# Performance work log

Hardware: AMD Instinct MI355X
Metric: run time of the kernel (lower is better)

## Reference

```python
import jax, jax.numpy as jnp
import numpy as np


def squash(x, axis=-1):
    # squared_norm * x / ((1 + squared_norm) * sqrt(squared_norm))
    sn = jnp.sum(x * x, axis=axis, keepdims=True)
    return sn * x / ((1.0 + sn) * jnp.sqrt(sn))


def conv2d(x, w, b, stride):
    out = jax.lax.conv_general_dilated(
        x, w, (stride, stride), 'VALID',
        dimension_numbers=('NCHW', 'OIHW', 'NCHW'))
    return out + b[None, :, None, None]


def setup_inputs() -> dict:
    key = jax.random.key(0)
    ks = jax.random.split(key, 8)
    B = 256
    s = 0.05
    data = jax.random.normal(ks[0], (B, 1, 28, 28), jnp.float32)
    conv_w = jax.random.normal(ks[1], (256, 1, 9, 9), jnp.float32) * s
    conv_b = jnp.zeros((256,), jnp.float32)
    pc_w = jax.random.normal(ks[2], (8, 32, 256, 9, 9), jnp.float32) * s  # 8 capsule convs
    pc_b = jnp.zeros((8, 32), jnp.float32)
    W = jax.random.normal(ks[3], (1, 1152, 10, 16, 8), jnp.float32)  # torch.randn init
    dec_w1 = jax.random.normal(ks[4], (512, 160), jnp.float32) * s
    dec_b1 = jnp.zeros((512,), jnp.float32)
    dec_w2 = jax.random.normal(ks[5], (1024, 512), jnp.float32) * s
    dec_b2 = jnp.zeros((1024,), jnp.float32)
    dec_w3 = jax.random.normal(ks[6], (784, 1024), jnp.float32) * s
    dec_b3 = jnp.zeros((784,), jnp.float32)
    return dict(data=data, conv_w=conv_w, conv_b=conv_b, pc_w=pc_w, pc_b=pc_b,
                W=W, dec_w1=dec_w1, dec_b1=dec_b1, dec_w2=dec_w2, dec_b2=dec_b2,
                dec_w3=dec_w3, dec_b3=dec_b3)


def reference(data, conv_w, conv_b, pc_w, pc_b, W,
              dec_w1, dec_b1, dec_w2, dec_b2, dec_w3, dec_b3):
    B = data.shape[0]
    # ConvLayer
    x = jax.nn.relu(conv2d(data, conv_w, conv_b, 1))        # [B,256,20,20]
    # PrimaryCaps: 8 separate convs == one conv with 8*32 output channels
    pw = pc_w.reshape(8 * 32, 256, 9, 9)
    pb = pc_b.reshape(8 * 32)
    u = conv2d(x, pw, pb, 2)                                # [B,256,6,6] == stack dim=1 of [B,8,32,6,6]
    u = u.reshape(B, 1152, 8)                               # matches torch .view(B, num_routes, -1)
    u = squash(u)                                           # over 8-dim capsule axis
    # DigitCaps: u_hat[b,r,c,o] = W[0,r,c,o,:] . u[b,r,:]
    u_hat = jnp.einsum('rcoi,bri->brco', W[0], u)           # [B,1152,10,16]
    b_ij = jnp.zeros((1, 1152, 10, 1), u_hat.dtype)         # shared across batch (as in torch)
    v_j = None
    for it in range(3):
        c = jax.nn.softmax(b_ij, axis=1)                    # softmax over routes
        s_j = jnp.sum(c * u_hat, axis=1, keepdims=True)     # [B,1,10,16]
        # NOTE: torch squash here acts on a trailing singleton dim -> elementwise
        # out = s^2 * s / ((1+s^2)*|s|) = s*|s|/(1+s^2)
        v_j = s_j * jnp.abs(s_j) / (1.0 + s_j * s_j)
        if it < 2:
            a = jnp.sum(u_hat * v_j, axis=3)                # agreement, [B,1152,10]
            b_ij = b_ij + jnp.mean(a, axis=0, keepdims=True)[..., None]
    output = v_j[:, 0, :, :, None]                          # [B,10,16,1] (v_j.squeeze(1) in torch layout)
    # Decoder
    classes = jnp.sqrt(jnp.sum(output ** 2, axis=2))        # [B,10,1]
    classes = jax.nn.softmax(classes, axis=0)               # dim=0 softmax (as in source)
    idx = jnp.argmax(classes[:, :, 0], axis=1)              # [B]
    masked = jnp.eye(10, dtype=output.dtype)[idx]           # [B,10]
    t = (output * masked[:, :, None, None]).reshape(B, -1)  # [B,160]
    h = jax.nn.relu(t @ dec_w1.T + dec_b1)
    h = jax.nn.relu(h @ dec_w2.T + dec_b2)
    recon = jax.nn.sigmoid(h @ dec_w3.T + dec_b3)
    reconstructions = recon.reshape(B, 1, 28, 28)
    return output, reconstructions, masked
```

## Files before the change

kernel.cpp:

```cpp
#include <hip/hip_runtime.h>
#include <math.h>

typedef __attribute__((ext_vector_type(8))) short short8;
typedef __attribute__((ext_vector_type(16))) float f32x16;
typedef unsigned short ushort_t;

static __device__ __forceinline__ unsigned short f2bf(float f) {
  unsigned int u = __float_as_uint(f);
  u += 0x7FFF + ((u >> 16) & 1);
  return (unsigned short)(u >> 16);
}
static __device__ __forceinline__ float bf2f(unsigned short h) {
  return __uint_as_float(((unsigned int)h) << 16);
}

__device__ __forceinline__ void gl2lds16(const void* g, void* l) {
  __builtin_amdgcn_global_load_lds(
      (const __attribute__((address_space(1))) unsigned int*)g,
      (__attribute__((address_space(3))) unsigned int*)l, 16, 0, 0);
}

__global__ __launch_bounds__(256) void acvt_kernel(const float* __restrict__ cw,
                                                   ushort_t* __restrict__ ah,
                                                   ushort_t* __restrict__ al) {
  int tid = blockIdx.x * 256 + threadIdx.x;
  if (tid >= 4608) return;
  int l = tid & 63;
  int ocg = (tid >> 6) & 7;
  int kc = tid >> 9;
  int oc = ocg * 32 + (l & 31);
  size_t obase = (size_t)tid * 8;
#pragma unroll
  for (int e = 0; e < 8; ++e) {
    int kwp = ((l >> 5) << 3) + e;
    float v = (kwp < 9) ? cw[oc * 81 + kc * 9 + kwp] : 0.f;
    unsigned short h = f2bf(v);
    ah[obase + e] = h;
    al[obase + e] = f2bf(v - bf2f(h));
  }
}

__global__ __launch_bounds__(256) void im2col_kernel(const float* __restrict__ data,
                                                     ushort_t* __restrict__ bh,
                                                     ushort_t* __restrict__ bl) {
  int idx16 = blockIdx.x * 256 + threadIdx.x;
  int kc = idx16 / 204800;
  int rem = idx16 - kc * 204800;
  int n = rem >> 1, half = rem & 1;
  int b = n / 400;
  int pos = n - b * 400;
  int ph = pos / 20, pw = pos - ph * 20;
  const float* src = data + b * 784 + (ph + kc) * 28 + pw + half * 8;
  size_t obase = (size_t)idx16 * 8;
#pragma unroll
  for (int e = 0; e < 8; ++e) {
    int kwp = half * 8 + e;
    float v = (kwp < 9) ? src[e] : 0.f;
    unsigned short h = f2bf(v);
    bh[obase + e] = h;
    bl[obase + e] = f2bf(v - bf2f(h));
  }
}

struct StageC {
  ushort_t ah[2][8][64][8];
  ushort_t al[2][8][64][8];
  ushort_t bh[2][2][64][8];
  ushort_t bl[2][2][64][8];
};
__global__ __launch_bounds__(256, 2) void cgemm_kernel(
    const ushort_t* __restrict__ Afh, const ushort_t* __restrict__ Afl,
    const ushort_t* __restrict__ Bfh, const ushort_t* __restrict__ Bfl,
    const float* __restrict__ cb, ushort_t* __restrict__ xTh,
    ushort_t* __restrict__ xTl) {
  __shared__ __align__(16) union { StageC st; float ep[256][33]; } L;
  const int t = threadIdx.x;
  const int l = t & 63;
  const int w = t >> 6;
  const int n0 = blockIdx.x * 64;

  f32x16 acc[2][2];
#pragma unroll
  for (int j = 0; j < 2; ++j)
#pragma unroll
    for (int nc = 0; nc < 2; ++nc)
#pragma unroll
      for (int r = 0; r < 16; ++r) acc[j][nc][r] = 0.f;

  auto stage = [&](int buf, int kc) {
#pragma unroll
    for (int q5 = 0; q5 < 5; ++q5) {
      int q = w * 5 + q5;
      if (q < 16) {
        int sp = q >> 3, ocg = q & 7;
        const ushort_t* src = (sp ? Afl : Afh) + ((size_t)(kc * 8 + ocg) * 64 + l) * 8;
        gl2lds16(src, sp ? &L.st.al[buf][ocg][0][0] : &L.st.ah[buf][ocg][0][0]);
      } else {
        int j = q - 16;
        int sp = j >> 1, nc = j & 1;
        const ushort_t* src =
            (sp ? Bfl : Bfh) +
            (((size_t)kc * 102400 + (n0 + nc * 32 + (l & 31))) * 2 + (l >> 5)) * 8;
        gl2lds16(src, sp ? &L.st.bl[buf][nc][0][0] : &L.st.bh[buf][nc][0][0]);
      }
    }
  };

  stage(0, 0);
  __syncthreads();
  int buf = 0;
  for (int kc = 0; kc < 9; ++kc) {
    if (kc < 8) stage(buf ^ 1, kc + 1);
    short8 a0h = *(const short8*)&L.st.ah[buf][2 * w + 0][l][0];
    short8 a1h = *(const short8*)&L.st.ah[buf][2 * w + 1][l][0];
    short8 a0l = *(const short8*)&L.st.al[buf][2 * w + 0][l][0];
    short8 a1l = *(const short8*)&L.st.al[buf][2 * w + 1][l][0];
#pragma unroll
    for (int nc = 0; nc < 2; ++nc) {
      short8 bh = *(const short8*)&L.st.bh[buf][nc][l][0];
      short8 bl = *(const short8*)&L.st.bl[buf][nc][l][0];
      acc[0][nc] = __builtin_amdgcn_mfma_f32_32x32x16_bf16(a0h, bh, acc[0][nc], 0, 0, 0);
      acc[0][nc] = __builtin_amdgcn_mfma_f32_32x32x16_bf16(a0h, bl, acc[0][nc], 0, 0, 0);
      acc[0][nc] = __builtin_amdgcn_mfma_f32_32x32x16_bf16(a0l, bh, acc[0][nc], 0, 0, 0);
      acc[1][nc] = __builtin_amdgcn_mfma_f32_32x32x16_bf16(a1h, bh, acc[1][nc], 0, 0, 0);
      acc[1][nc] = __builtin_amdgcn_mfma_f32_32x32x16_bf16(a1h, bl, acc[1][nc], 0, 0, 0);
      acc[1][nc] = __builtin_amdgcn_mfma_f32_32x32x16_bf16(a1l, bh, acc[1][nc], 0, 0, 0);
    }
    __syncthreads();
    buf ^= 1;
  }

  for (int nc = 0; nc < 2; ++nc) {
    __syncthreads();
#pragma unroll
    for (int j = 0; j < 2; ++j)
#pragma unroll
      for (int r = 0; r < 16; ++r) {
        int row = w * 64 + j * 32 + (r & 3) + 8 * (r >> 2) + ((l >> 5) << 2);
        L.ep[row][l & 31] = fmaxf(acc[j][nc][r] + cb[row], 0.f);
      }
    __syncthreads();
    int nl = t >> 3, ocr = (t & 7) * 32;
    size_t ng = (size_t)(n0 + nc * 32 + nl);
#pragma unroll
    for (int q8 = 0; q8 < 4; ++q8) {
      short8 sh, sl;
#pragma unroll
      for (int e = 0; e < 8; ++e) {
        float vv = L.ep[ocr + q8 * 8 + e][nl];
        unsigned short h = f2bf(vv);
        sh[e] = (short)h;
        sl[e] = (short)f2bf(vv - bf2f(h));
      }
      *(short8*)&xTh[ng * 256 + ocr + q8 * 8] = sh;
      *(short8*)&xTl[ng * 256 + ocr + q8 * 8] = sl;
    }
  }
}

__global__ __launch_bounds__(256) void wcvt_kernel(const float* __restrict__ pw,
                                                   ushort_t* __restrict__ ah,
                                                   ushort_t* __restrict__ al) {
  int tid = blockIdx.x * 256 + threadIdx.x;
  int l = tid & 63;
  int ocg = (tid >> 6) & 7;
  int kc = tid >> 9;
  int oc = ocg * 32 + (l & 31);
  size_t obase = (size_t)tid * 8;
#pragma unroll
  for (int e = 0; e < 8; ++e) {
    int k = kc * 16 + ((l >> 5) << 3) + e;
    int kh = k / 2304;
    int r = k - kh * 2304;
    int kw = r >> 8, ic = r & 255;
    float v = pw[((size_t)oc * 256 + ic) * 81 + kh * 9 + kw];
    unsigned short h = f2bf(v);
    ah[obase + e] = h;
    al[obase + e] = f2bf(v - bf2f(h));
  }
}

__global__ __launch_bounds__(256, 2) void pgemm_kernel(
    const ushort_t* __restrict__ Agh, const ushort_t* __restrict__ Agl,
    const ushort_t* __restrict__ Xh, const ushort_t* __restrict__ Xl,
    float* __restrict__ part) {
  __shared__ __align__(16) ushort_t sA[2][2][2][4][64][8];
  __shared__ __align__(16) ushort_t sB[2][2][2][4][64][8];
  const int t = threadIdx.x;
  const int l = t & 63;
  const int w = t >> 6;
  const int wm = w >> 1, wn = w & 1;
  const int m0 = blockIdx.y;
  const int n0 = blockIdx.x * 128;
  const int zk = blockIdx.z;
  const int kcb = zk * 162;

  int n = n0 + w * 32 + (l & 31);
  int b_ = n / 36;
  int pos = n - b_ * 36;
  int ph = pos / 6, pww = pos - ph * 6;
  size_t pbase = (((size_t)b_ * 20 + 2 * ph) * 20 + 2 * pww) * 256 + ((l >> 5) << 3);

  const int sw = w >> 1, klw = w & 1;
  const ushort_t* Asrc = sw ? Agl : Agh;
  const size_t aoff0 = (((size_t)(kcb + klw) * 8 + m0 * 4) * 64 + l) * 8;

  f32x16 acc[2][2];
#pragma unroll
  for (int j = 0; j < 2; ++j)
#pragma unroll
    for (int j2 = 0; j2 < 2; ++j2)
#pragma unroll
      for (int r = 0; r < 16; ++r) acc[j][j2][r] = 0.f;

  auto koff = [](int kc) {
    int kh = (unsigned)kc / 144u;
    int r = kc - kh * 144;
    return ((kh * 20 + (r >> 4)) << 8) + ((r & 15) << 4);
  };
  auto stage = [&](int buf, int step) {
    size_t ao = aoff0 + (size_t)step * 8192;
#pragma unroll
    for (int j = 0; j < 4; ++j)
      gl2lds16(Asrc + ao + j * 512, &sA[buf][sw][klw][j][0][0]);
    int kc0 = kcb + 2 * step;
    int o0 = koff(kc0), o1 = koff(kc0 + 1);
    gl2lds16(Xh + pbase + o0, &sB[buf][0][0][w][0][0]);
    gl2lds16(Xh + pbase + o1, &sB[buf][0][1][w][0][0]);
    gl2lds16(Xl + pbase + o0, &sB[buf][1][0][w][0][0]);
    gl2lds16(Xl + pbase + o1, &sB[buf][1][1][w][0][0]);
  };

  stage(0, 0);
  __syncthreads();
  int buf = 0;
  for (int step = 0; step < 81; ++step) {
    if (step + 1 < 81) stage(buf ^ 1, step + 1);
#pragma unroll
    for (int kl = 0; kl < 2; ++kl) {
      short8 a0h = *(const short8*)&sA[buf][0][kl][wm * 2 + 0][l][0];
      short8 a1h = *(const short8*)&sA[buf][0][kl][wm * 2 + 1][l][0];
      short8 a0l = *(const short8*)&sA[buf][1][kl][wm * 2 + 0][l][0];
      short8 a1l = *(const short8*)&sA[buf][1][kl][wm * 2 + 1][l][0];
      short8 b0h = *(const short8*)&sB[buf][0][kl][wn * 2 + 0][l][0];
      short8 b1h = *(const short8*)&sB[buf][0][kl][wn * 2 + 1][l][0];
      short8 b0l = *(const short8*)&sB[buf][1][kl][wn * 2 + 0][l][0];
      short8 b1l = *(const short8*)&sB[buf][1][kl][wn * 2 + 1][l][0];
      acc[0][0] = __builtin_amdgcn_mfma_f32_32x32x16_bf16(a0h, b0h, acc[0][0], 0, 0, 0);
      acc[0][0] = __builtin_amdgcn_mfma_f32_32x32x16_bf16(a0h, b0l, acc[0][0], 0, 0, 0);
      acc[0][0] = __builtin_amdgcn_mfma_f32_32x32x16_bf16(a0l, b0h, acc[0][0], 0, 0, 0);
      acc[0][1] = __builtin_amdgcn_mfma_f32_32x32x16_bf16(a0h, b1h, acc[0][1], 0, 0, 0);
      acc[0][1] = __builtin_amdgcn_mfma_f32_32x32x16_bf16(a0h, b1l, acc[0][1], 0, 0, 0);
      acc[0][1] = __builtin_amdgcn_mfma_f32_32x32x16_bf16(a0l, b1h, acc[0][1], 0, 0, 0);
      acc[1][0] = __builtin_amdgcn_mfma_f32_32x32x16_bf16(a1h, b0h, acc[1][0], 0, 0, 0);
      acc[1][0] = __builtin_amdgcn_mfma_f32_32x32x16_bf16(a1h, b0l, acc[1][0], 0, 0, 0);
      acc[1][0] = __builtin_amdgcn_mfma_f32_32x32x16_bf16(a1l, b0h, acc[1][0], 0, 0, 0);
      acc[1][1] = __builtin_amdgcn_mfma_f32_32x32x16_bf16(a1h, b1h, acc[1][1], 0, 0, 0);
      acc[1][1] = __builtin_amdgcn_mfma_f32_32x32x16_bf16(a1h, b1l, acc[1][1], 0, 0, 0);
      acc[1][1] = __builtin_amdgcn_mfma_f32_32x32x16_bf16(a1l, b1h, acc[1][1], 0, 0, 0);
    }
    __syncthreads();
    buf ^= 1;
  }

#pragma unroll
  for (int j = 0; j < 2; ++j)
#pragma unroll
    for (int j2 = 0; j2 < 2; ++j2) {
      int ocb = m0 * 128 + wm * 64 + j * 32;
      int nb = n0 + wn * 64 + j2 * 32 + (l & 31);
#pragma unroll
      for (int r = 0; r < 16; ++r) {
        int row = (r & 3) + 8 * (r >> 2) + ((l >> 5) << 2);
        part[((size_t)(zk * 256 + ocb + row)) * 9216 + nb] = acc[j][j2][r];
      }
    }
}

__global__ __launch_bounds__(256) void ured_kernel(const float* __restrict__ part,
                                                   const float* __restrict__ pb,
                                                   float* __restrict__ u) {
  int tid = blockIdx.x * 256 + threadIdx.x;
  int oc = tid / 9216;
  int n = tid - oc * 9216;
  float s = pb[oc];
#pragma unroll
  for (int z = 0; z < 8; ++z) s += part[((size_t)z * 256 + oc) * 9216 + n];
  int b = n / 36;
  int pos = n - b * 36;
  u[(size_t)b * 9216 + oc * 36 + pos] = s;
}

__global__ __launch_bounds__(256) void sqcvt_kernel(const float* __restrict__ u,
                                                    ushort_t* __restrict__ ubh,
                                                    ushort_t* __restrict__ ubl,
                                                    ushort_t* __restrict__ uth,
                                                    ushort_t* __restrict__ utl) {
  int kt = blockIdx.x, bt = blockIdx.y;
  int k0 = kt * 64, b0 = bt * 64;
  __shared__ ushort_t lh[64][66], ll_[64][66];
  int t = threadIdx.x;
#pragma unroll
  for (int jj = 0; jj < 2; ++jj) {
    int item = t + 256 * jj;
    int g = item & 7, bl = item >> 3;
    int b = b0 + bl, kb = k0 + g * 8;
    const float4* p4 = reinterpret_cast<const float4*>(u + (size_t)b * 9216 + kb);
    float4 v0 = p4[0], v1 = p4[1];
    float va[8] = {v0.x, v0.y, v0.z, v0.w, v1.x, v1.y, v1.z, v1.w};
    float sn = 0.f;
#pragma unroll
    for (int e = 0; e < 8; ++e) sn += va[e] * va[e];
    float f = sn / ((1.f + sn) * sqrtf(sn));
    short8 sh, sl;
#pragma unroll
    for (int e = 0; e < 8; ++e) {
      float vv = va[e] * f;
      unsigned short h = f2bf(vv);
      unsigned short lo = f2bf(vv - bf2f(h));
      sh[e] = (short)h;
      sl[e] = (short)lo;
      lh[g * 8 + e][bl] = h;
      ll_[g * 8 + e][bl] = lo;
    }
    *(short8*)&ubh[(size_t)b * 9216 + kb] = sh;
    *(short8*)&ubl[(size_t)b * 9216 + kb] = sl;
  }
  __syncthreads();
  int kl = t >> 2, br = (t & 3) * 16;
#pragma unroll
  for (int q = 0; q < 2; ++q) {
    short8 sh, sl;
#pragma unroll
    for (int e = 0; e < 8; ++e) {
      sh[e] = (short)lh[kl][br + q * 8 + e];
      sl[e] = (short)ll_[kl][br + q * 8 + e];
    }
    *(short8*)&uth[(size_t)(k0 + kl) * 256 + b0 + br + q * 8] = sh;
    *(short8*)&utl[(size_t)(k0 + kl) * 256 + b0 + br + q * 8] = sl;
  }
}

__global__ void zero_kernel(float* __restrict__ p, int n) {
  int i = blockIdx.x * 256 + threadIdx.x;
  if (i < n) p[i] = 0.f;
}

__global__ __launch_bounds__(256) void softmax_c_kernel(const float* __restrict__ bp,
                                                        float* __restrict__ c) {
  int cls = blockIdx.x;
  int t = threadIdx.x;
  __shared__ float red[256];
  float m = -1e30f;
  for (int r = t; r < 1152; r += 256) m = fmaxf(m, bp[r * 10 + cls]);
  red[t] = m;
  __syncthreads();
  for (int s = 128; s > 0; s >>= 1) {
    if (t < s) red[t] = fmaxf(red[t], red[t + s]);
    __syncthreads();
  }
  m = red[0];
  __syncthreads();
  float sum = 0.f;
  for (int r = t; r < 1152; r += 256) sum += expf(bp[r * 10 + cls] - m);
  red[t] = sum;
  __syncthreads();
  for (int s = 128; s > 0; s >>= 1) {
    if (t < s) red[t] += red[t + s];
    __syncthreads();
  }
  float den = red[0];
  for (int r = t; r < 1152; r += 256) c[r * 10 + cls] = expf(bp[r * 10 + cls] - m) / den;
}

__global__ __launch_bounds__(256) void wcb_kernel(const float* __restrict__ W,
                                                  const float* __restrict__ c,
                                                  ushort_t* __restrict__ wh,
                                                  ushort_t* __restrict__ wl) {
  int tid = blockIdx.x * 256 + threadIdx.x;
  int col = tid / 1152;
  int kg = tid - col * 1152;
  int cls = col >> 4, o = col & 15;
  float cc = c[kg * 10 + cls];
  const float4* wp = reinterpret_cast<const float4*>(W + (((size_t)kg * 10 + cls) * 16 + o) * 8);
  float4 w0 = wp[0], w1 = wp[1];
  float wa[8] = {w0.x, w0.y, w0.z, w0.w, w1.x, w1.y, w1.z, w1.w};
  short8 sh, sl;
#pragma unroll
  for (int e = 0; e < 8; ++e) {
    float vv = wa[e] * cc;
    unsigned short h = f2bf(vv);
    sh[e] = (short)h;
    sl[e] = (short)f2bf(vv - bf2f(h));
  }
  *(short8*)&wh[(size_t)col * 9216 + kg * 8] = sh;
  *(short8*)&wl[(size_t)col * 9216 + kg * 8] = sl;
}

__global__ __launch_bounds__(64, 1) void smfma_kernel(
    const ushort_t* __restrict__ ubh, const ushort_t* __restrict__ ubl,
    const ushort_t* __restrict__ wh, const ushort_t* __restrict__ wl,
    float* __restrict__ s_part) {
  int ks = blockIdx.x, bt = blockIdx.y;
  __shared__ __align__(16) ushort_t Ah[4][2][64][8], Al[4][2][64][8];
  __shared__ __align__(16) ushort_t Bh[4][5][64][8], Bl[4][5][64][8];
  int l = threadIdx.x;
  int k0 = ks * 64;
#pragma unroll
  for (int kc = 0; kc < 4; ++kc) {
#pragma unroll
    for (int mh = 0; mh < 2; ++mh) {
      size_t ao = (size_t)(bt * 64 + mh * 32 + (l & 31)) * 9216 + k0 + kc * 16 + ((l >> 5) << 3);
      gl2lds16(ubh + ao, &Ah[kc][mh][0][0]);
      gl2lds16(ubl + ao, &Al[kc][mh][0][0]);
    }
#pragma unroll
    for (int cf = 0; cf < 5; ++cf) {
      size_t bo = (size_t)(cf * 32 + (l & 31)) * 9216 + k0 + kc * 16 + ((l >> 5) << 3);
      gl2lds16(wh + bo, &Bh[kc][cf][0][0]);
      gl2lds16(wl + bo, &Bl[kc][cf][0][0]);
    }
  }
  __builtin_amdgcn_s_waitcnt(0);
  __syncthreads();
  f32x16 acc[2][5];
#pragma unroll
  for (int m = 0; m < 2; ++m)
#pragma unroll
    for (int cf = 0; cf < 5; ++cf)
#pragma unroll
      for (int r = 0; r < 16; ++r) acc[m][cf][r] = 0.f;
#pragma unroll
  for (int kc = 0; kc < 4; ++kc) {
    short8 a0h = *(const short8*)&Ah[kc][0][l][0];
    short8 a1h = *(const short8*)&Ah[kc][1][l][0];
    short8 a0l = *(const short8*)&Al[kc][0][l][0];
    short8 a1l = *(const short8*)&Al[kc][1][l][0];
#pragma unroll
    for (int cf = 0; cf < 5; ++cf) {
      short8 bh = *(const short8*)&Bh[kc][cf][l][0];
      short8 bl = *(const short8*)&Bl[kc][cf][l][0];
      acc[0][cf] = __builtin_amdgcn_mfma_f32_32x32x16_bf16(a0h, bh, acc[0][cf], 0, 0, 0);
      acc[0][cf] = __builtin_amdgcn_mfma_f32_32x32x16_bf16(a0h, bl, acc[0][cf], 0, 0, 0);
      acc[0][cf] = __builtin_amdgcn_mfma_f32_32x32x16_bf16(a0l, bh, acc[0][cf], 0, 0, 0);
      acc[1][cf] = __builtin_amdgcn_mfma_f32_32x32x16_bf16(a1h, bh, acc[1][cf], 0, 0, 0);
      acc[1][cf] = __builtin_amdgcn_mfma_f32_32x32x16_bf16(a1h, bl, acc[1][cf], 0, 0, 0);
      acc[1][cf] = __builtin_amdgcn_mfma_f32_32x32x16_bf16(a1l, bh, acc[1][cf], 0, 0, 0);
    }
  }
#pragma unroll
  for (int mh = 0; mh < 2; ++mh)
#pragma unroll
    for (int cf = 0; cf < 5; ++cf)
#pragma unroll
      for (int r = 0; r < 16; ++r) {
        int row = bt * 64 + mh * 32 + (r & 3) + 8 * (r >> 2) + ((l >> 5) << 2);
        s_part[((size_t)ks * 256 + row) * 160 + cf * 32 + (l & 31)] = acc[mh][cf][r];
      }
}

__global__ __launch_bounds__(256) void reduce_v_kernel(
    const float* __restrict__ s_part, float* __restrict__ v,
    ushort_t* __restrict__ vth, ushort_t* __restrict__ vtl,
    float* __restrict__ out, int write_out) {
  int i = blockIdx.x * 256 + threadIdx.x;
  float s0 = 0.f, s1 = 0.f, s2 = 0.f, s3 = 0.f;
#pragma unroll 4
  for (int ks = 0; ks < 144; ks += 4) {
    s0 += s_part[(size_t)ks * 40960 + i];
    s1 += s_part[(size_t)(ks + 1) * 40960 + i];
    s2 += s_part[(size_t)(ks + 2) * 40960 + i];
    s3 += s_part[(size_t)(ks + 3) * 40960 + i];
  }
  float s = (s0 + s1) + (s2 + s3);
  float val = s * fabsf(s) / (1.f + s * s);
  v[i] = val;
  int b = i / 160, col = i - b * 160;
  unsigned short h = f2bf(val);
  vth[col * 256 + b] = h;
  vtl[col * 256 + b] = f2bf(val - bf2f(h));
  if (write_out) out[i] = val;
}

struct StageT {
  ushort_t ah[2][2][2][64][8];
  ushort_t al[2][2][2][64][8];
  ushort_t bh[2][2][5][64][8];
  ushort_t bl[2][2][5][64][8];
};
__global__ __launch_bounds__(256) void tmfma_kernel(
    const ushort_t* __restrict__ uth, const ushort_t* __restrict__ utl,
    const ushort_t* __restrict__ vth, const ushort_t* __restrict__ vtl,
    float* __restrict__ Tp) {
  __shared__ __align__(16) union { StageT st; float red[2][32][160]; } L;
  int mt = blockIdx.x, kh = blockIdx.y;
  int t = threadIdx.x;
  int l = t & 63, w = t >> 6;
  int wm = w & 1, wk = w >> 1;
  int m0 = mt * 64;

  auto stage = [&](int buf, int step) {
    int kb = kh * 128 + wk * 64 + step * 16;
    size_t ao = (size_t)(m0 + wm * 32 + (l & 31)) * 256 + kb + ((l >> 5) << 3);
    gl2lds16(uth + ao, &L.st.ah[buf][wk][wm][0][0]);
    gl2lds16(utl + ao, &L.st.al[buf][wk][wm][0][0]);
#pragma unroll
    for (int q = 0; q < 5; ++q) {
      int qq = wm * 5 + q;
      int cf = qq >> 1, sp = qq & 1;
      size_t bo = (size_t)(cf * 32 + (l & 31)) * 256 + kb + ((l >> 5) << 3);
      gl2lds16((sp ? vtl : vth) + bo,
               sp ? &L.st.bl[buf][wk][cf][0][0] : &L.st.bh[buf][wk][cf][0][0]);
    }
  };

  f32x16 acc[5];
#pragma unroll
  for (int cf = 0; cf < 5; ++cf)
#pragma unroll
    for (int r = 0; r < 16; ++r) acc[cf][r] = 0.f;

  stage(0, 0);
  __syncthreads();
  int buf = 0;
  for (int step = 0; step < 4; ++step) {
    if (step < 3) stage(buf ^ 1, step + 1);
    short8 ah = *(const short8*)&L.st.ah[buf][wk][wm][l][0];
    short8 al = *(const short8*)&L.st.al[buf][wk][wm][l][0];
#pragma unroll
    for (int cf = 0; cf < 5; ++cf) {
      short8 bh = *(const short8*)&L.st.bh[buf][wk][cf][l][0];
      short8 bl = *(const short8*)&L.st.bl[buf][wk][cf][l][0];
      acc[cf] = __builtin_amdgcn_mfma_f32_32x32x16_bf16(ah, bh, acc[cf], 0, 0, 0);
      acc[cf] = __builtin_amdgcn_mfma_f32_32x32x16_bf16(ah, bl, acc[cf], 0, 0, 0);
      acc[cf] = __builtin_amdgcn_mfma_f32_32x32x16_bf16(al, bh, acc[cf], 0, 0, 0);
    }
    __syncthreads();
    buf ^= 1;
  }
  if (wk == 1) {
#pragma unroll
    for (int cf = 0; cf < 5; ++cf)
#pragma unroll
      for (int r = 0; r < 16; ++r) {
        int row = (r & 3) + 8 * (r >> 2) + ((l >> 5) << 2);
        L.red[wm][row][cf * 32 + (l & 31)] = acc[cf][r];
      }
  }
  __syncthreads();
  if (wk == 0) {
    const float scl = 1.f / 256.f;
#pragma unroll
    for (int cf = 0; cf < 5; ++cf)
#pragma unroll
      for (int r = 0; r < 16; ++r) {
        int row = (r & 3) + 8 * (r >> 2) + ((l >> 5) << 2);
        int col = cf * 32 + (l & 31);
        float val = (acc[cf][r] + L.red[wm][row][col]) * scl;
        Tp[((size_t)kh * 9216 + m0 + wm * 32 + row) * 160 + col] = val;
      }
  }
}

__global__ __launch_bounds__(256) void bp_update_kernel(const float* __restrict__ W,
                                                        const float* __restrict__ Tp,
                                                        float* __restrict__ bp) {
  int idx = blockIdx.x * 256 + threadIdx.x;
  if (idx >= 11520) return;
  int r = idx / 10, cls = idx % 10;
  const float* wp = W + (size_t)idx * 128;
  const float* T1 = Tp + 1474560;
  float s = 0.f;
#pragma unroll
  for (int o = 0; o < 16; ++o)
#pragma unroll
    for (int i = 0; i < 8; ++i) {
      size_t ti = (size_t)(r * 8 + i) * 160 + cls * 16 + o;
      s = fmaf(wp[o * 8 + i], Tp[ti] + T1[ti], s);
    }
  bp[idx] += s;
}

__global__ __launch_bounds__(256) void mask_kernel(const float* __restrict__ v,
                                                   float* __restrict__ masked,
                                                   int* __restrict__ bi_out,
                                                   float* __restrict__ tsel) {
  __shared__ float cls_s[256][10];
  __shared__ float colmax[10], colden[10];
  int t = threadIdx.x;
  float cl[10];
  for (int c = 0; c < 10; ++c) {
    float sum = 0.f;
    for (int o = 0; o < 16; ++o) {
      float q = v[t * 160 + c * 16 + o];
      sum += q * q;
    }
    cl[c] = sqrtf(sum);
    cls_s[t][c] = cl[c];
  }
  __syncthreads();
  if (t < 10) {
    float m = -1e30f;
    for (int b = 0; b < 256; ++b) m = fmaxf(m, cls_s[b][t]);
    float d = 0.f;
    for (int b = 0; b < 256; ++b) d += expf(cls_s[b][t] - m);
    colmax[t] = m;
    colden[t] = d;
  }
  __syncthreads();
  float best = -1e30f;
  int bi = 0;
  for (int c = 0; c < 10; ++c) {
    float p = expf(cl[c] - colmax[c]) / colden[c];
    if (p > best) { best = p; bi = c; }
  }
  for (int c = 0; c < 10; ++c) masked[t * 10 + c] = (c == bi) ? 1.f : 0.f;
  bi_out[t] = bi;
  for (int o = 0; o < 16; ++o) tsel[t * 16 + o] = v[t * 160 + bi * 16 + o];
}

__global__ __launch_bounds__(256) void fc1s_kernel(const float* __restrict__ tsel,
                                                   const int* __restrict__ bi,
                                                   const float* __restrict__ w1,
                                                   const float* __restrict__ b1,
                                                   float* __restrict__ h1) {
  int b = blockIdx.x;
  int t = threadIdx.x;
  __shared__ float ts[16];
  __shared__ int sbi;
  if (t < 16) ts[t] = tsel[b * 16 + t];
  if (t == 0) sbi = bi[b];
  __syncthreads();
  for (int j = t; j < 512; j += 256) {
    const float* wp = w1 + (size_t)j * 160 + sbi * 16;
    float a = b1[j];
#pragma unroll
    for (int o = 0; o < 16; ++o) a = fmaf(ts[o], wp[o], a);
    h1[(size_t)b * 512 + j] = fmaxf(a, 0.f);
  }
}

template <int ACT>
__global__ __launch_bounds__(256) void fc_kernel(const float* __restrict__ in,
                                                 const float* __restrict__ w,
                                                 const float* __restrict__ bias,
                                                 float* __restrict__ out, int K, int N) {
  int jt = blockIdx.x, bt = blockIdx.y;
  __shared__ float in_s[16][33];
  __shared__ float w_s[64][33];
  int t = threadIdx.x;
  int jl = t & 63, bq = t >> 6;
  float acc[4] = {0, 0, 0, 0};
  for (int k0 = 0; k0 < K; k0 += 32) {
    __syncthreads();
    for (int q = t; q < 512; q += 256) {
      int bb = q >> 5, kk = q & 31;
      in_s[bb][kk] = in[(size_t)(bt * 16 + bb) * K + k0 + kk];
    }
    for (int q = t; q < 2048; q += 256) {
      int jj = q >> 5, kk = q & 31;
      int jg = jt * 64 + jj;
      w_s[jj][kk] = (jg < N) ? w[(size_t)jg * K + k0 + kk] : 0.f;
    }
    __syncthreads();
#pragma unroll
    for (int kk = 0; kk < 32; ++kk) {
      float wv = w_s[jl][kk];
#pragma unroll
      for (int m = 0; m < 4; ++m) acc[m] = fmaf(in_s[bq * 4 + m][kk], wv, acc[m]);
    }
  }
  int jg = jt * 64 + jl;
  if (jg < N) {
    float bv = bias[jg];
    for (int m = 0; m < 4; ++m) {
      float r = acc[m] + bv;
      if (ACT == 0)
        r = fmaxf(r, 0.f);
      else
        r = 1.f / (1.f + expf(-r));
      out[(size_t)(bt * 16 + bq * 4 + m) * N + jg] = r;
    }
  }
}

extern "C" void kernel_launch(void* const* d_in, const int* in_sizes, int n_in,
                              void* d_out, int out_size, void* d_ws, size_t ws_size,
                              hipStream_t stream) {
  const float* data  = (const float*)d_in[0];
  const float* convw = (const float*)d_in[1];
  const float* convb = (const float*)d_in[2];
  const float* pcw   = (const float*)d_in[3];
  const float* pcb   = (const float*)d_in[4];
  const float* W     = (const float*)d_in[5];
  const float* w1    = (const float*)d_in[6];
  const float* b1    = (const float*)d_in[7];
  const float* w2    = (const float*)d_in[8];
  const float* b2    = (const float*)d_in[9];
  const float* w3    = (const float*)d_in[10];
  const float* b3    = (const float*)d_in[11];
  float* out = (float*)d_out;

  char* wsb = (char*)d_ws;
  size_t off = 0;
  auto allocb = [&](size_t bytes) {
    void* p = wsb + off;
    off += (bytes + 255) & ~(size_t)255;
    return p;
  };
  float* part = (float*)allocb(75497472);
  ushort_t* Bfh = (ushort_t*)part;
  ushort_t* Bfl = Bfh + 14745600;
  ushort_t* ubh = (ushort_t*)part;
  ushort_t* ubl = ubh + 2359296;
  ushort_t* uth = ubl + 2359296;
  ushort_t* utl = uth + 2359296;
  float* u    = (float*)allocb(9437184);
  float* v    = (float*)allocb(163840);
  float* bp   = (float*)allocb(46080);
  float* c    = (float*)allocb(46080);
  ushort_t* WCbh = (ushort_t*)allocb(2949120);
  ushort_t* WCbl = (ushort_t*)allocb(2949120);
  ushort_t* vth  = (ushort_t*)allocb(81920);
  ushort_t* vtl  = (ushort_t*)allocb(81920);
  int*   bi   = (int*)allocb(1024);
  float* tsel = (float*)allocb(16384);
  float* s_part = (float*)allocb(23592960);
  float* Tp = s_part;
  float* h1 = s_part;
  float* h2 = s_part + 131072;
  ushort_t* Agh = (ushort_t*)allocb(10616832);
  ushort_t* Agl = (ushort_t*)allocb(10616832);
  ushort_t* Afch = (ushort_t*)allocb(147456);
  ushort_t* Afcl = (ushort_t*)allocb(147456);
  ushort_t* xTh = (ushort_t*)allocb(52428800);
  ushort_t* xTl = (ushort_t*)allocb(52428800);
  if (ws_size < off) return;

  acvt_kernel<<<18, 256, 0, stream>>>(convw, Afch, Afcl);
  im2col_kernel<<<7200, 256, 0, stream>>>(data, Bfh, Bfl);
  cgemm_kernel<<<1600, 256, 0, stream>>>(Afch, Afcl, Bfh, Bfl, convb, xTh, xTl);
  wcvt_kernel<<<2592, 256, 0, stream>>>(pcw, Agh, Agl);
  pgemm_kernel<<<dim3(72, 2, 8), 256, 0, stream>>>(Agh, Agl, xTh, xTl, part);
  ured_kernel<<<9216, 256, 0, stream>>>(part, pcb, u);
  sqcvt_kernel<<<dim3(144, 4), 256, 0, stream>>>(u, ubh, ubl, uth, utl);
  zero_kernel<<<45, 256, 0, stream>>>(bp, 11520);

  for (int it = 0; it < 3; ++it) {
    softmax_c_kernel<<<10, 256, 0, stream>>>(bp, c);
    wcb_kernel<<<720, 256, 0, stream>>>(W, c, WCbh, WCbl);
    smfma_kernel<<<dim3(144, 4), 64, 0, stream>>>(ubh, ubl, WCbh, WCbl, s_part);
    reduce_v_kernel<<<160, 256, 0, stream>>>(s_part, v, vth, vtl, out, it == 2 ? 1 : 0);
    if (it < 2) {
      tmfma_kernel<<<dim3(144, 2), 256, 0, stream>>>(uth, utl, vth, vtl, Tp);
      bp_update_kernel<<<45, 256, 0, stream>>>(W, Tp, bp);
    }
  }

  mask_kernel<<<1, 256, 0, stream>>>(v, out + 241664, bi, tsel);
  fc1s_kernel<<<256, 256, 0, stream>>>(tsel, bi, w1, b1, h1);
  fc_kernel<0><<<dim3(16, 16), 256, 0, stream>>>(h1, w2, b2, h2, 512, 1024);
  fc_kernel<1><<<dim3(13, 16), 256, 0, stream>>>(h2, w3, b3, out + 40960, 1024, 784);
}
```

Before: 997.6 us.

## Fuse im2col into conv GEMM, deepen pgemm pipeline, split routing MFMA kernels

The conv GEMM now builds its bf16 hi/lo B fragments straight from the input image in registers, so the separate im2col kernel and its large intermediate buffer are gone. The A operand is read from global memory instead of staged through LDS. The primary-capsule GEMM moves to a prefetch distance of two stages, with explicit vmcnt waits, raw barriers and raised priority around the MFMA block. The routing smfma and tmfma kernels are rewritten as small 64-thread blocks that read operands directly from global memory, and the class-fragment and column-tile dimensions move into the grid. This removes the split-K partial sum in bp_update, in exchange for more blocks and less operand reuse across them.

Result: faster. 904.6 us (-9.3%).

```diff
diff --git a/kernel.cpp b/kernel.cpp
--- a/kernel.cpp
+++ b/kernel.cpp
@@ -40,44 +40,29 @@
   }
 }
 
-__global__ __launch_bounds__(256) void im2col_kernel(const float* __restrict__ data,
-                                                     ushort_t* __restrict__ bh,
-                                                     ushort_t* __restrict__ bl) {
-  int idx16 = blockIdx.x * 256 + threadIdx.x;
-  int kc = idx16 / 204800;
-  int rem = idx16 - kc * 204800;
-  int n = rem >> 1, half = rem & 1;
-  int b = n / 400;
-  int pos = n - b * 400;
-  int ph = pos / 20, pw = pos - ph * 20;
-  const float* src = data + b * 784 + (ph + kc) * 28 + pw + half * 8;
-  size_t obase = (size_t)idx16 * 8;
-#pragma unroll
-  for (int e = 0; e < 8; ++e) {
-    int kwp = half * 8 + e;
-    float v = (kwp < 9) ? src[e] : 0.f;
-    unsigned short h = f2bf(v);
-    bh[obase + e] = h;
-    bl[obase + e] = f2bf(v - bf2f(h));
-  }
-}
-
-struct StageC {
-  ushort_t ah[2][8][64][8];
-  ushort_t al[2][8][64][8];
-  ushort_t bh[2][2][64][8];
-  ushort_t bl[2][2][64][8];
-};
 __global__ __launch_bounds__(256, 2) void cgemm_kernel(
     const ushort_t* __restrict__ Afh, const ushort_t* __restrict__ Afl,
-    const ushort_t* __restrict__ Bfh, const ushort_t* __restrict__ Bfl,
-    const float* __restrict__ cb, ushort_t* __restrict__ xTh,
-    ushort_t* __restrict__ xTl) {
-  __shared__ __align__(16) union { StageC st; float ep[256][33]; } L;
+    const float* __restrict__ data, const float* __restrict__ cb,
+    ushort_t* __restrict__ xTh, ushort_t* __restrict__ xTl) {
+  __shared__ float ep[256][33];
   const int t = threadIdx.x;
   const int l = t & 63;
   const int w = t >> 6;
   const int n0 = blockIdx.x * 64;
+  const int half = l >> 5;
+
+  const float* rowp0;
+  const float* rowp1;
+  {
+    int n = n0 + (l & 31);
+    int b = n / 400, pos = n - b * 400;
+    int ph = pos / 20, pw = pos - ph * 20;
+    rowp0 = data + b * 784 + ph * 28 + pw;
+    n = n0 + 32 + (l & 31);
+    b = n / 400; pos = n - b * 400;
+    ph = pos / 20; pw = pos - ph * 20;
+    rowp1 = data + b * 784 + ph * 28 + pw;
+  }
 
   f32x16 acc[2][2];
 #pragma unroll
@@ -87,47 +72,30 @@
 #pragma unroll
       for (int r = 0; r < 16; ++r) acc[j][nc][r] = 0.f;
 
-  auto stage = [&](int buf, int kc) {
-#pragma unroll
-    for (int q5 = 0; q5 < 5; ++q5) {
-      int q = w * 5 + q5;
-      if (q < 16) {
-        int sp = q >> 3, ocg = q & 7;
-        const ushort_t* src = (sp ? Afl : Afh) + ((size_t)(kc * 8 + ocg) * 64 + l) * 8;
-        gl2lds16(src, sp ? &L.st.al[buf][ocg][0][0] : &L.st.ah[buf][ocg][0][0]);
-      } else {
-        int j = q - 16;
-        int sp = j >> 1, nc = j & 1;
-        const ushort_t* src =
-            (sp ? Bfl : Bfh) +
-            (((size_t)kc * 102400 + (n0 + nc * 32 + (l & 31))) * 2 + (l >> 5)) * 8;
-        gl2lds16(src, sp ? &L.st.bl[buf][nc][0][0] : &L.st.bh[buf][nc][0][0]);
+  for (int kc = 0; kc < 9; ++kc) {
+    short8 a0h = *(const short8*)&Afh[((size_t)(kc * 8 + 2 * w + 0) * 64 + l) * 8];
+    short8 a1h = *(const short8*)&Afh[((size_t)(kc * 8 + 2 * w + 1) * 64 + l) * 8];
+    short8 a0l = *(const short8*)&Afl[((size_t)(kc * 8 + 2 * w + 0) * 64 + l) * 8];
+    short8 a1l = *(const short8*)&Afl[((size_t)(kc * 8 + 2 * w + 1) * 64 + l) * 8];
+#pragma unroll
+    for (int nc = 0; nc < 2; ++nc) {
+      const float* rp = (nc ? rowp1 : rowp0) + kc * 28;
+      short8 bh8, bl8;
+#pragma unroll
+      for (int e = 0; e < 8; ++e) {
+        int kwp = half * 8 + e;
+        float v = (kwp < 9) ? rp[kwp] : 0.f;
+        unsigned short h = f2bf(v);
+        bh8[e] = (short)h;
+        bl8[e] = (short)f2bf(v - bf2f(h));
       }
-    }
-  };
-
-  stage(0, 0);
-  __syncthreads();
-  int buf = 0;
-  for (int kc = 0; kc < 9; ++kc) {
-    if (kc < 8) stage(buf ^ 1, kc + 1);
-    short8 a0h = *(const short8*)&L.st.ah[buf][2 * w + 0][l][0];
-    short8 a1h = *(const short8*)&L.st.ah[buf][2 * w + 1][l][0];
-    short8 a0l = *(const short8*)&L.st.al[buf][2 * w + 0][l][0];
-    short8 a1l = *(const short8*)&L.st.al[buf][2 * w + 1][l][0];
-#pragma unroll
-    for (int nc = 0; nc < 2; ++nc) {
-      short8 bh = *(const short8*)&L.st.bh[buf][nc][l][0];
-      short8 bl = *(const short8*)&L.st.bl[buf][nc][l][0];
-      acc[0][nc] = __builtin_amdgcn_mfma_f32_32x32x16_bf16(a0h, bh, acc[0][nc], 0, 0, 0);
-      acc[0][nc] = __builtin_amdgcn_mfma_f32_32x32x16_bf16(a0h, bl, acc[0][nc], 0, 0, 0);
-      acc[0][nc] = __builtin_amdgcn_mfma_f32_32x32x16_bf16(a0l, bh, acc[0][nc], 0, 0, 0);
-      acc[1][nc] = __builtin_amdgcn_mfma_f32_32x32x16_bf16(a1h, bh, acc[1][nc], 0, 0, 0);
-      acc[1][nc] = __builtin_amdgcn_mfma_f32_32x32x16_bf16(a1h, bl, acc[1][nc], 0, 0, 0);
-      acc[1][nc] = __builtin_amdgcn_mfma_f32_32x32x16_bf16(a1l, bh, acc[1][nc], 0, 0, 0);
-    }
-    __syncthreads();
-    buf ^= 1;
+      acc[0][nc] = __builtin_amdgcn_mfma_f32_32x32x16_bf16(a0h, bh8, acc[0][nc], 0, 0, 0);
+      acc[0][nc] = __builtin_amdgcn_mfma_f32_32x32x16_bf16(a0h, bl8, acc[0][nc], 0, 0, 0);
+      acc[0][nc] = __builtin_amdgcn_mfma_f32_32x32x16_bf16(a0l, bh8, acc[0][nc], 0, 0, 0);
+      acc[1][nc] = __builtin_amdgcn_mfma_f32_32x32x16_bf16(a1h, bh8, acc[1][nc], 0, 0, 0);
+      acc[1][nc] = __builtin_amdgcn_mfma_f32_32x32x16_bf16(a1h, bl8, acc[1][nc], 0, 0, 0);
+      acc[1][nc] = __builtin_amdgcn_mfma_f32_32x32x16_bf16(a1l, bh8, acc[1][nc], 0, 0, 0);
+    }
   }
 
   for (int nc = 0; nc < 2; ++nc) {
@@ -137,7 +105,7 @@
 #pragma unroll
       for (int r = 0; r < 16; ++r) {
         int row = w * 64 + j * 32 + (r & 3) + 8 * (r >> 2) + ((l >> 5) << 2);
-        L.ep[row][l & 31] = fmaxf(acc[j][nc][r] + cb[row], 0.f);
+        ep[row][l & 31] = fmaxf(acc[j][nc][r] + cb[row], 0.f);
       }
     __syncthreads();
     int nl = t >> 3, ocr = (t & 7) * 32;
@@ -147,7 +115,7 @@
       short8 sh, sl;
 #pragma unroll
       for (int e = 0; e < 8; ++e) {
-        float vv = L.ep[ocr + q8 * 8 + e][nl];
+        float vv = ep[ocr + q8 * 8 + e][nl];
         unsigned short h = f2bf(vv);
         sh[e] = (short)h;
         sl[e] = (short)f2bf(vv - bf2f(h));
@@ -232,10 +200,16 @@
   };
 
   stage(0, 0);
-  __syncthreads();
-  int buf = 0;
+  stage(1, 1);
   for (int step = 0; step < 81; ++step) {
-    if (step + 1 < 81) stage(buf ^ 1, step + 1);
+    if (step < 80)
+      asm volatile("s_waitcnt vmcnt(8)" ::: "memory");
+    else
+      asm volatile("s_waitcnt vmcnt(0)" ::: "memory");
+    __builtin_amdgcn_sched_barrier(0);
+    __builtin_amdgcn_s_barrier();
+    const int buf = step & 1;
+    __builtin_amdgcn_s_setprio(1);
 #pragma unroll
     for (int kl = 0; kl < 2; ++kl) {
       short8 a0h = *(const short8*)&sA[buf][0][kl][wm * 2 + 0][l][0];
@@ -259,8 +233,10 @@
       acc[1][1] = __builtin_amdgcn_mfma_f32_32x32x16_bf16(a1h, b1l, acc[1][1], 0, 0, 0);
       acc[1][1] = __builtin_amdgcn_mfma_f32_32x32x16_bf16(a1l, b1h, acc[1][1], 0, 0, 0);
     }
-    __syncthreads();
-    buf ^= 1;
+    __builtin_amdgcn_s_setprio(0);
+    __builtin_amdgcn_s_barrier();
+    __builtin_amdgcn_sched_barrier(0);
+    if (step < 79) stage(buf, step + 2);
   }
 
 #pragma unroll
@@ -397,66 +373,41 @@
   *(short8*)&wl[(size_t)col * 9216 + kg * 8] = sl;
 }
 
-__global__ __launch_bounds__(64, 1) void smfma_kernel(
+__global__ __launch_bounds__(64) void smfma_kernel(
     const ushort_t* __restrict__ ubh, const ushort_t* __restrict__ ubl,
     const ushort_t* __restrict__ wh, const ushort_t* __restrict__ wl,
     float* __restrict__ s_part) {
-  int ks = blockIdx.x, bt = blockIdx.y;
-  __shared__ __align__(16) ushort_t Ah[4][2][64][8], Al[4][2][64][8];
-  __shared__ __align__(16) ushort_t Bh[4][5][64][8], Bl[4][5][64][8];
+  int ks = blockIdx.x, bt = blockIdx.y, cf = blockIdx.z;
   int l = threadIdx.x;
   int k0 = ks * 64;
+  int kf = ((l >> 5) << 3);
+  f32x16 acc[2];
+#pragma unroll
+  for (int m = 0; m < 2; ++m)
+#pragma unroll
+    for (int r = 0; r < 16; ++r) acc[m][r] = 0.f;
 #pragma unroll
   for (int kc = 0; kc < 4; ++kc) {
+    size_t bo = (size_t)(cf * 32 + (l & 31)) * 9216 + k0 + kc * 16 + kf;
+    short8 bh = *(const short8*)&wh[bo];
+    short8 bl = *(const short8*)&wl[bo];
 #pragma unroll
     for (int mh = 0; mh < 2; ++mh) {
-      size_t ao = (size_t)(bt * 64 + mh * 32 + (l & 31)) * 9216 + k0 + kc * 16 + ((l >> 5) << 3);
-      gl2lds16(ubh + ao, &Ah[kc][mh][0][0]);
-      gl2lds16(ubl + ao, &Al[kc][mh][0][0]);
-    }
-#pragma unroll
-    for (int cf = 0; cf < 5; ++cf) {
-      size_t bo = (size_t)(cf * 32 + (l & 31)) * 9216 + k0 + kc * 16 + ((l >> 5) << 3);
-      gl2lds16(wh + bo, &Bh[kc][cf][0][0]);
-      gl2lds16(wl + bo, &Bl[kc][cf][0][0]);
-    }
-  }
-  __builtin_amdgcn_s_waitcnt(0);
-  __syncthreads();
-  f32x16 acc[2][5];
-#pragma unroll
-  for (int m = 0; m < 2; ++m)
-#pragma unroll
-    for (int cf = 0; cf < 5; ++cf)
-#pragma unroll
-      for (int r = 0; r < 16; ++r) acc[m][cf][r] = 0.f;
-#pragma unroll
-  for (int kc = 0; kc < 4; ++kc) {
-    short8 a0h = *(const short8*)&Ah[kc][0][l][0];
-    short8 a1h = *(const short8*)&Ah[kc][1][l][0];
-    short8 a0l = *(const short8*)&Al[kc][0][l][0];
-    short8 a1l = *(const short8*)&Al[kc][1][l][0];
-#pragma unroll
-    for (int cf = 0; cf < 5; ++cf) {
-      short8 bh = *(const short8*)&Bh[kc][cf][l][0];
-      short8 bl = *(const short8*)&Bl[kc][cf][l][0];
-      acc[0][cf] = __builtin_amdgcn_mfma_f32_32x32x16_bf16(a0h, bh, acc[0][cf], 0, 0, 0);
-      acc[0][cf] = __builtin_amdgcn_mfma_f32_32x32x16_bf16(a0h, bl, acc[0][cf], 0, 0, 0);
-      acc[0][cf] = __builtin_amdgcn_mfma_f32_32x32x16_bf16(a0l, bh, acc[0][cf], 0, 0, 0);
-      acc[1][cf] = __builtin_amdgcn_mfma_f32_32x32x16_bf16(a1h, bh, acc[1][cf], 0, 0, 0);
-      acc[1][cf] = __builtin_amdgcn_mfma_f32_32x32x16_bf16(a1h, bl, acc[1][cf], 0, 0, 0);
-      acc[1][cf] = __builtin_amdgcn_mfma_f32_32x32x16_bf16(a1l, bh, acc[1][cf], 0, 0, 0);
+      size_t ao = (size_t)(bt * 64 + mh * 32 + (l & 31)) * 9216 + k0 + kc * 16 + kf;
+      short8 ah = *(const short8*)&ubh[ao];
+      short8 al = *(const short8*)&ubl[ao];
+      acc[mh] = __builtin_amdgcn_mfma_f32_32x32x16_bf16(ah, bh, acc[mh], 0, 0, 0);
+      acc[mh] = __builtin_amdgcn_mfma_f32_32x32x16_bf16(ah, bl, acc[mh], 0, 0, 0);
+      acc[mh] = __builtin_amdgcn_mfma_f32_32x32x16_bf16(al, bh, acc[mh], 0, 0, 0);
     }
   }
 #pragma unroll
   for (int mh = 0; mh < 2; ++mh)
 #pragma unroll
-    for (int cf = 0; cf < 5; ++cf)
-#pragma unroll
-      for (int r = 0; r < 16; ++r) {
-        int row = bt * 64 + mh * 32 + (r & 3) + 8 * (r >> 2) + ((l >> 5) << 2);
-        s_part[((size_t)ks * 256 + row) * 160 + cf * 32 + (l & 31)] = acc[mh][cf][r];
-      }
+    for (int r = 0; r < 16; ++r) {
+      int row = bt * 64 + mh * 32 + (r & 3) + 8 * (r >> 2) + ((l >> 5) << 2);
+      s_part[((size_t)ks * 256 + row) * 160 + cf * 32 + (l & 31)] = acc[mh][r];
+    }
 }
 
 __global__ __launch_bounds__(256) void reduce_v_kernel(
@@ -482,102 +433,49 @@
   if (write_out) out[i] = val;
 }
 
-struct StageT {
-  ushort_t ah[2][2][2][64][8];
-  ushort_t al[2][2][2][64][8];
-  ushort_t bh[2][2][5][64][8];
-  ushort_t bl[2][2][5][64][8];
-};
-__global__ __launch_bounds__(256) void tmfma_kernel(
+__global__ __launch_bounds__(64) void tmfma_kernel(
     const ushort_t* __restrict__ uth, const ushort_t* __restrict__ utl,
     const ushort_t* __restrict__ vth, const ushort_t* __restrict__ vtl,
-    float* __restrict__ Tp) {
-  __shared__ __align__(16) union { StageT st; float red[2][32][160]; } L;
-  int mt = blockIdx.x, kh = blockIdx.y;
-  int t = threadIdx.x;
-  int l = t & 63, w = t >> 6;
-  int wm = w & 1, wk = w >> 1;
-  int m0 = mt * 64;
-
-  auto stage = [&](int buf, int step) {
-    int kb = kh * 128 + wk * 64 + step * 16;
-    size_t ao = (size_t)(m0 + wm * 32 + (l & 31)) * 256 + kb + ((l >> 5) << 3);
-    gl2lds16(uth + ao, &L.st.ah[buf][wk][wm][0][0]);
-    gl2lds16(utl + ao, &L.st.al[buf][wk][wm][0][0]);
-#pragma unroll
-    for (int q = 0; q < 5; ++q) {
-      int qq = wm * 5 + q;
-      int cf = qq >> 1, sp = qq & 1;
-      size_t bo = (size_t)(cf * 32 + (l & 31)) * 256 + kb + ((l >> 5) << 3);
-      gl2lds16((sp ? vtl : vth) + bo,
-               sp ? &L.st.bl[buf][wk][cf][0][0] : &L.st.bh[buf][wk][cf][0][0]);
-    }
-  };
-
-  f32x16 acc[5];
-#pragma unroll
-  for (int cf = 0; cf < 5; ++cf)
-#pragma unroll
-    for (int r = 0; r < 16; ++r) acc[cf][r] = 0.f;
-
-  stage(0, 0);
-  __syncthreads();
-  int buf = 0;
-  for (int step = 0; step < 4; ++step) {
-    if (step < 3) stage(buf ^ 1, step + 1);
-    short8 ah = *(const short8*)&L.st.ah[buf][wk][wm][l][0];
-    short8 al = *(const short8*)&L.st.al[buf][wk][wm][l][0];
-#pragma unroll
-    for (int cf = 0; cf < 5; ++cf) {
-      short8 bh = *(const short8*)&L.st.bh[buf][wk][cf][l][0];
-      short8 bl = *(const short8*)&L.st.bl[buf][wk][cf][l][0];
-      acc[cf] = __builtin_amdgcn_mfma_f32_32x32x16_bf16(ah, bh, acc[cf], 0, 0, 0);
-      acc[cf] = __builtin_amdgcn_mfma_f32_32x32x16_bf16(ah, bl, acc[cf], 0, 0, 0);
-      acc[cf] = __builtin_amdgcn_mfma_f32_32x32x16_bf16(al, bh, acc[cf], 0, 0, 0);
-    }
-    __syncthreads();
-    buf ^= 1;
-  }
-  if (wk == 1) {
-#pragma unroll
-    for (int cf = 0; cf < 5; ++cf)
-#pragma unroll
-      for (int r = 0; r < 16; ++r) {
-        int row = (r & 3) + 8 * (r >> 2) + ((l >> 5) << 2);
-        L.red[wm][row][cf * 32 + (l & 31)] = acc[cf][r];
-      }
-  }
-  __syncthreads();
-  if (wk == 0) {
-    const float scl = 1.f / 256.f;
-#pragma unroll
-    for (int cf = 0; cf < 5; ++cf)
-#pragma unroll
-      for (int r = 0; r < 16; ++r) {
-        int row = (r & 3) + 8 * (r >> 2) + ((l >> 5) << 2);
-        int col = cf * 32 + (l & 31);
-        float val = (acc[cf][r] + L.red[wm][row][col]) * scl;
-        Tp[((size_t)kh * 9216 + m0 + wm * 32 + row) * 160 + col] = val;
-      }
+    float* __restrict__ T) {
+  int mt = blockIdx.x, cf = blockIdx.y;
+  int l = threadIdx.x;
+  int m0 = mt * 32;
+  int bf = ((l >> 5) << 3);
+  f32x16 acc;
+#pragma unroll
+  for (int r = 0; r < 16; ++r) acc[r] = 0.f;
+  for (int step = 0; step < 16; ++step) {
+    size_t ao = (size_t)(m0 + (l & 31)) * 256 + step * 16 + bf;
+    size_t bo = (size_t)(cf * 32 + (l & 31)) * 256 + step * 16 + bf;
+    short8 ah = *(const short8*)&uth[ao];
+    short8 al = *(const short8*)&utl[ao];
+    short8 bh = *(const short8*)&vth[bo];
+    short8 bl = *(const short8*)&vtl[bo];
+    acc = __builtin_amdgcn_mfma_f32_32x32x16_bf16(ah, bh, acc, 0, 0, 0);
+    acc = __builtin_amdgcn_mfma_f32_32x32x16_bf16(ah, bl, acc, 0, 0, 0);
+    acc = __builtin_amdgcn_mfma_f32_32x32x16_bf16(al, bh, acc, 0, 0, 0);
+  }
+  const float scl = 1.f / 256.f;
+#pragma unroll
+  for (int r = 0; r < 16; ++r) {
+    int row = (r & 3) + 8 * (r >> 2) + ((l >> 5) << 2);
+    T[(size_t)(m0 + row) * 160 + cf * 32 + (l & 31)] = acc[r] * scl;
   }
 }
 
 __global__ __launch_bounds__(256) void bp_update_kernel(const float* __restrict__ W,
-                                                        const float* __restrict__ Tp,
+                                                        const float* __restrict__ T,
                                                         float* __restrict__ bp) {
   int idx = blockIdx.x * 256 + threadIdx.x;
   if (idx >= 11520) return;
   int r = idx / 10, cls = idx % 10;
   const float* wp = W + (size_t)idx * 128;
-  const float* T1 = Tp + 1474560;
   float s = 0.f;
 #pragma unroll
   for (int o = 0; o < 16; ++o)
 #pragma unroll
-    for (int i = 0; i < 8; ++i) {
-      size_t ti = (size_t)(r * 8 + i) * 160 + cls * 16 + o;
-      s = fmaf(wp[o * 8 + i], Tp[ti] + T1[ti], s);
-    }
+    for (int i = 0; i < 8; ++i)
+      s = fmaf(wp[o * 8 + i], T[(size_t)(r * 8 + i) * 160 + cls * 16 + o], s);
   bp[idx] += s;
 }
 
@@ -709,8 +607,6 @@
     return p;
   };
   float* part = (float*)allocb(75497472);
-  ushort_t* Bfh = (ushort_t*)part;
-  ushort_t* Bfl = Bfh + 14745600;
   ushort_t* ubh = (ushort_t*)part;
   ushort_t* ubl = ubh + 2359296;
   ushort_t* uth = ubl + 2359296;
@@ -726,7 +622,7 @@
   int*   bi   = (int*)allocb(1024);
   float* tsel = (float*)allocb(16384);
   float* s_part = (float*)allocb(23592960);
-  float* Tp = s_part;
+  float* T  = s_part;
   float* h1 = s_part;
   float* h2 = s_part + 131072;
   ushort_t* Agh = (ushort_t*)allocb(10616832);
@@ -738,8 +634,7 @@
   if (ws_size < off) return;
 
   acvt_kernel<<<18, 256, 0, stream>>>(convw, Afch, Afcl);
-  im2col_kernel<<<7200, 256, 0, stream>>>(data, Bfh, Bfl);
-  cgemm_kernel<<<1600, 256, 0, stream>>>(Afch, Afcl, Bfh, Bfl, convb, xTh, xTl);
+  cgemm_kernel<<<1600, 256, 0, stream>>>(Afch, Afcl, data, convb, xTh, xTl);
   wcvt_kernel<<<2592, 256, 0, stream>>>(pcw, Agh, Agl);
   pgemm_kernel<<<dim3(72, 2, 8), 256, 0, stream>>>(Agh, Agl, xTh, xTl, part);
   ured_kernel<<<9216, 256, 0, stream>>>(part, pcb, u);
@@ -749,11 +644,11 @@
   for (int it = 0; it < 3; ++it) {
     softmax_c_kernel<<<10, 256, 0, stream>>>(bp, c);
     wcb_kernel<<<720, 256, 0, stream>>>(W, c, WCbh, WCbl);
-    smfma_kernel<<<dim3(144, 4), 64, 0, stream>>>(ubh, ubl, WCbh, WCbl, s_part);
+    smfma_kernel<<<dim3(144, 4, 5), 64, 0, stream>>>(ubh, ubl, WCbh, WCbl, s_part);
     reduce_v_kernel<<<160, 256, 0, stream>>>(s_part, v, vth, vtl, out, it == 2 ? 1 : 0);
     if (it < 2) {
-      tmfma_kernel<<<dim3(144, 2), 256, 0, stream>>>(uth, utl, vth, vtl, Tp);
-      bp_update_kernel<<<45, 256, 0, stream>>>(W, Tp, bp);
+      tmfma_kernel<<<dim3(288, 5), 64, 0, stream>>>(uth, utl, vth, vtl, T);
+      bp_update_kernel<<<45, 256, 0, stream>>>(W, T, bp);
     }
   }
 
```
